# Optimization experiments

Measured on AMD Instinct MI355X. Metric: run time of the kernel, lower is better.

Reference implementation:

```python
import jax, jax.numpy as jnp
import numpy as np

N_EMBED = 384
N_HEADS = 6
HEAD_SIZE = 64


def setup_inputs() -> dict:
    key = jax.random.key(0)
    ks = jax.random.split(key, 6)
    B, T = 16, 1024
    x = jax.random.normal(ks[0], (B, T, N_EMBED), dtype=jnp.float32)
    s = 1.0 / np.sqrt(N_EMBED)
    wq = jax.random.normal(ks[1], (N_HEADS, N_EMBED, HEAD_SIZE), dtype=jnp.float32) * s
    wk = jax.random.normal(ks[2], (N_HEADS, N_EMBED, HEAD_SIZE), dtype=jnp.float32) * s
    wv = jax.random.normal(ks[3], (N_HEADS, N_EMBED, HEAD_SIZE), dtype=jnp.float32) * s
    wp = jax.random.normal(ks[4], (N_EMBED, N_EMBED), dtype=jnp.float32) * s
    bp = jnp.zeros((N_EMBED,), dtype=jnp.float32)
    return {"x": x, "wq": wq, "wk": wk, "wv": wv, "wp": wp, "bp": bp}


def reference(x, wq, wk, wv, wp, bp):
    B, T, C = x.shape
    # per-head projections: [B,H,T,D]
    q = jnp.einsum('btc,hcd->bhtd', x, wq)
    k = jnp.einsum('btc,hcd->bhtd', x, wk)
    v = jnp.einsum('btc,hcd->bhtd', x, wv)
    # NOTE: original scales by 1/sqrt(C) with C = embed dim (384), no causal mask
    scores = jnp.einsum('bhtd,bhsd->bhts', q, k) / jnp.sqrt(jnp.asarray(C, x.dtype))
    weights = jax.nn.softmax(scores, axis=-1)  # dropout = identity (eval)
    out = jnp.einsum('bhts,bhsd->bhtd', weights, v)
    # concat heads -> [B,T,H*D]
    out = out.transpose(0, 2, 1, 3).reshape(B, T, -1)
    return out @ wp.T + bp
```

## Files before the change

### kernel.cpp

```cpp
#include <hip/hip_runtime.h>
#include <hip/hip_bf16.h>

#define Hn 6
#define Tn 1024
#define Cn 384
#define Dn 64
#define Bn 16
#define Mn (Bn*Tn)
#define QSCALE 0.07362222f

typedef __attribute__((ext_vector_type(8)))  short s16x8;
typedef __attribute__((ext_vector_type(16))) float f32x16;

__device__ __forceinline__ void gl_lds16(const void* g, void* l) {
  __builtin_amdgcn_global_load_lds(
      (const __attribute__((address_space(1))) unsigned int*)g,
      (__attribute__((address_space(3))) unsigned int*)l, 16, 0, 0);
}
__device__ __forceinline__ unsigned pk2f(float a, float b) {
  __hip_bfloat162 h = __float22bfloat162_rn(make_float2(a, b));
  union { __hip_bfloat162 h; unsigned u; } cv; cv.h = h; return cv.u;
}
__device__ __forceinline__ f32x16 mfma32(s16x8 a, s16x8 b, f32x16 c) {
  return __builtin_amdgcn_mfma_f32_32x32x16_bf16(a, b, c, 0, 0, 0);
}

__global__ __launch_bounds__(256) void convert_all(
    const float* __restrict__ x, const float* __restrict__ wq,
    const float* __restrict__ wk, const float* __restrict__ wv,
    const float* __restrict__ wp,
    __hip_bfloat16* __restrict__ xb, __hip_bfloat16* __restrict__ wt,
    __hip_bfloat16* __restrict__ wpb)
{
  const int bid = blockIdx.x, t = threadIdx.x;
  if (bid < 18) {
    __shared__ float lt[64][65];
    const int mat = bid / Hn, hh = bid % Hn;
    const float* src = (mat == 0 ? wq : mat == 1 ? wk : wv) + (size_t)hh * (Cn*Dn);
    __hip_bfloat16* dst = wt + (size_t)mat * (Hn*Dn*Cn) + (size_t)hh * (Dn*Cn);
    const float sc = (mat == 0) ? QSCALE : 1.0f;
    for (int ct = 0; ct < 6; ++ct) {
      __syncthreads();
      #pragma unroll
      for (int ps = 0; ps < 4; ++ps) {
        int idx = ps*256 + t;
        int cl = idx >> 4, s4 = idx & 15;
        float4 v = *reinterpret_cast<const float4*>(src + (size_t)(ct*64 + cl)*Dn + s4*4);
        lt[cl][s4*4+0] = v.x * sc; lt[cl][s4*4+1] = v.y * sc;
        lt[cl][s4*4+2] = v.z * sc; lt[cl][s4*4+3] = v.w * sc;
      }
      __syncthreads();
      const int dd = t >> 2, cq = t & 3;
      #pragma unroll
      for (int i = 0; i < 16; ++i)
        dst[(size_t)dd*Cn + ct*64 + cq*16 + i] = __float2bfloat16(lt[cq*16 + i][dd]);
    }
  } else if (bid < 90) {
    const size_t base = (size_t)(bid - 18) * 2048 + (size_t)t * 8;
    float4 a = *reinterpret_cast<const float4*>(wp + base);
    float4 b = *reinterpret_cast<const float4*>(wp + base + 4);
    uint4 r; r.x = pk2f(a.x,a.y); r.y = pk2f(a.z,a.w); r.z = pk2f(b.x,b.y); r.w = pk2f(b.z,b.w);
    *reinterpret_cast<uint4*>((char*)wpb + base*2) = r;
  } else {
    const size_t base = (size_t)(bid - 90) * 2048 + (size_t)t * 8;
    float4 a = *reinterpret_cast<const float4*>(x + base);
    float4 b = *reinterpret_cast<const float4*>(x + base + 4);
    uint4 r; r.x = pk2f(a.x,a.y); r.y = pk2f(a.z,a.w); r.z = pk2f(b.x,b.y); r.w = pk2f(b.z,b.w);
    *reinterpret_cast<uint4*>((char*)xb + base*2) = r;
  }
}

__global__ __launch_bounds__(256) void qkv_proj(
    const __hip_bfloat16* __restrict__ xb, const __hip_bfloat16* __restrict__ wt,
    __hip_bfloat16* __restrict__ qo, __hip_bfloat16* __restrict__ ko,
    __hip_bfloat16* __restrict__ vto)
{
  __shared__ __align__(16) char sm[8192];
  const int t = threadIdx.x, lane = t & 63, w = t >> 6;
  const int hi = lane >> 5, nl = lane & 31;
  const int wr = w >> 1, wc = w & 1;
  const int m0 = blockIdx.x * 64;
  const int mat = blockIdx.y / Hn, h = blockIdx.y % Hn;
  const __hip_bfloat16* wb = wt + (size_t)mat*(Hn*Dn*Cn) + (size_t)h*(Dn*Cn);

  const int mrow = wr*32 + nl;
  const int nrow = wc*32 + nl;
  f32x16 acc = {};
  for (int k0 = 0; k0 < Cn; k0 += 32) {
    __syncthreads();
    #pragma unroll
    for (int c = 0; c < 2; ++c) {
      const int off = w*2048 + c*1024 + lane*16;
      const char* src;
      if (off < 4096) {
        const int row = off >> 6, sl = (off >> 4) & 3;
        src = (const char*)(xb + (size_t)(m0 + row)*Cn + k0) + ((sl ^ (row & 3)) * 16);
      } else {
        const int o2 = off - 4096;
        const int row = o2 >> 6, sl = (o2 >> 4) & 3;
        src = (const char*)(wb + (size_t)row*Cn + k0) + ((sl ^ (row & 3)) * 16);
      }
      gl_lds16(src, sm + w*2048 + c*1024);
    }
    __syncthreads();
    #pragma unroll
    for (int kk = 0; kk < 2; ++kk) {
      s16x8 a  = *reinterpret_cast<const s16x8*>(sm + mrow*64 + (((2*kk + hi) ^ (mrow & 3)) * 16));
      s16x8 bb = *reinterpret_cast<const s16x8*>(sm + 4096 + nrow*64 + (((2*kk + hi) ^ (nrow & 3)) * 16));
      acc = mfma32(a, bb, acc);
    }
  }
  const int d = wc*32 + nl;
  if (mat < 2) {
    __hip_bfloat16* op = (mat == 0) ? qo : ko;
    #pragma unroll
    for (int r = 0; r < 16; ++r) {
      const int ml = wr*32 + (r & 3) + 8*(r >> 2) + 4*hi;
      const int M = m0 + ml, bI = M >> 10, tl = M & 1023;
      op[(((size_t)bI*Hn + h)*Tn + tl)*Dn + d] = __float2bfloat16(acc[r]);
    }
  } else {
    #pragma unroll
    for (int rq = 0; rq < 4; ++rq) {
      const int ml = wr*32 + 8*rq + 4*hi;
      const int M = m0 + ml, bI = M >> 10, tl = M & 1023;
      const unsigned u0 = pk2f(acc[rq*4+0], acc[rq*4+1]);
      const unsigned u1 = pk2f(acc[rq*4+2], acc[rq*4+3]);
      const unsigned long long v = ((unsigned long long)u1 << 32) | u0;
      *reinterpret_cast<unsigned long long*>(
          (char*)vto + ((((size_t)bI*Hn + h)*Dn + d)*Tn + tl)*2) = v;
    }
  }
}

__global__ __launch_bounds__(256) void attn_fwd(
    const __hip_bfloat16* __restrict__ qb, const __hip_bfloat16* __restrict__ kb,
    const __hip_bfloat16* __restrict__ vtb, __hip_bfloat16* __restrict__ ao)
{
  __shared__ __align__(16) char smem[16384];
  const int t = threadIdx.x, lane = t & 63, w = t >> 6;
  const int hi = lane >> 5, qm = lane & 31;
  const int l7 = lane & 7;
  const int bh = blockIdx.x >> 3, qt = blockIdx.x & 7;
  const int b = bh / Hn, h = bh % Hn;

  const int qrow = qt*128 + w*32 + qm;
  const __hip_bfloat16* qrp = qb + ((size_t)bh*Tn + qrow)*Dn;
  s16x8 qf[4];
  #pragma unroll
  for (int hh = 0; hh < 4; ++hh)
    qf[hh] = *reinterpret_cast<const s16x8*>(qrp + hh*16 + hi*8);

  const size_t kbase = (size_t)bh * Tn * Dn;
  const size_t vbase = (size_t)bh * Dn * Tn;

  f32x16 oacc[2] = {};
  float lsum = 0.f;

  for (int kt = 0; kt < 16; ++kt) {
    __syncthreads();
    #pragma unroll
    for (int c = 0; c < 4; ++c) {
      const int off = w*4096 + c*1024 + lane*16;
      const char* src;
      if (off < 8192) {
        const int row = off >> 7, sl = (off >> 4) & 7;
        src = (const char*)(kb + kbase + (size_t)(kt*64 + row)*Dn) + ((sl ^ (row & 7)) * 16);
      } else {
        const int o2 = off - 8192;
        const int row = o2 >> 7, sl = (o2 >> 4) & 7;
        src = (const char*)(vtb + vbase + (size_t)row*Tn + kt*64) + ((sl ^ (row & 7)) * 16);
      }
      gl_lds16(src, smem + w*4096 + c*1024);
    }
    __syncthreads();

    f32x16 sacc[2] = {};
    #pragma unroll
    for (int ts = 0; ts < 2; ++ts) {
      const int srow = ts*32 + qm;
      #pragma unroll
      for (int hh = 0; hh < 4; ++hh) {
        s16x8 ka = *reinterpret_cast<const s16x8*>(
            smem + srow*128 + (((2*hh + hi) ^ l7) * 16));
        sacc[ts] = mfma32(ka, qf[hh], sacc[ts]);
      }
    }
    #pragma unroll
    for (int ts = 0; ts < 2; ++ts)
      #pragma unroll
      for (int r = 0; r < 16; ++r) { float p = exp2f(sacc[ts][r]); sacc[ts][r] = p; lsum += p; }

    #pragma unroll
    for (int m = 0; m < 4; ++m) {
      const int ts = m >> 1, rb = 8*(m & 1);
      const unsigned A0 = pk2f(sacc[ts][rb+0], sacc[ts][rb+1]);
      const unsigned A1 = pk2f(sacc[ts][rb+2], sacc[ts][rb+3]);
      const unsigned B0 = pk2f(sacc[ts][rb+4], sacc[ts][rb+5]);
      const unsigned B1 = pk2f(sacc[ts][rb+6], sacc[ts][rb+7]);
      const unsigned s0 = hi ? A0 : B0;
      const unsigned s1 = hi ? A1 : B1;
      const unsigned r0 = __shfl_xor(s0, 32);
      const unsigned r1 = __shfl_xor(s1, 32);
      union { unsigned u[4]; s16x8 v; } fr;
      fr.u[0] = hi ? r0 : A0;  fr.u[1] = hi ? r1 : A1;
      fr.u[2] = hi ? B0 : r0;  fr.u[3] = hi ? B1 : r1;
      #pragma unroll
      for (int dt = 0; dt < 2; ++dt) {
        const int drow = dt*32 + qm;
        s16x8 va = *reinterpret_cast<const s16x8*>(
            smem + 8192 + drow*128 + (((2*m + hi) ^ l7) * 16));
        oacc[dt] = mfma32(va, fr.v, oacc[dt]);
      }
    }
  }

  lsum += __shfl_xor(lsum, 32);
  const float inv = 1.0f / lsum;

  __syncthreads();
  const int qloc = w*32 + qm;
  #pragma unroll
  for (int dt = 0; dt < 2; ++dt)
    #pragma unroll
    for (int rq = 0; rq < 4; ++rq) {
      const unsigned u0 = pk2f(oacc[dt][rq*4+0]*inv, oacc[dt][rq*4+1]*inv);
      const unsigned u1 = pk2f(oacc[dt][rq*4+2]*inv, oacc[dt][rq*4+3]*inv);
      const unsigned long long v = ((unsigned long long)u1 << 32) | u0;
      *reinterpret_cast<unsigned long long*>(
          smem + qloc*128 + (((4*dt + rq) ^ (qm & 7)) * 16) + 8*hi) = v;
    }
  __syncthreads();
  {
    const int qr = t >> 1, half = t & 1;
    char* dst = (char*)ao + ((size_t)(b*Tn + qt*128 + qr))*(Cn*2) + (h*Dn + half*32)*2;
    #pragma unroll
    for (int sl = 0; sl < 4; ++sl) {
      uint4 v = *reinterpret_cast<const uint4*>(
          smem + qr*128 + (((half*4 + sl) ^ (qr & 7)) * 16));
      *reinterpret_cast<uint4*>(dst + sl*16) = v;
    }
  }
}

__global__ __launch_bounds__(256) void out_proj(
    const __hip_bfloat16* __restrict__ ab, const __hip_bfloat16* __restrict__ wpb,
    const float* __restrict__ bp, float* __restrict__ out)
{
  __shared__ __align__(16) char sm[8192];
  const int t = threadIdx.x, lane = t & 63, w = t >> 6;
  const int hi = lane >> 5, nl = lane & 31;
  const int wr = w >> 1, wc = w & 1;
  const int m0 = blockIdx.x * 64;
  const int n0 = blockIdx.y * 64;

  const int mrow = wr*32 + nl;
  const int nrow = wc*32 + nl;
  f32x16 acc = {};
  for (int k0 = 0; k0 < Cn; k0 += 32) {
    __syncthreads();
    #pragma unroll
    for (int c = 0; c < 2; ++c) {
      const int off = w*2048 + c*1024 + lane*16;
      const char* src;
      if (off < 4096) {
        const int row = off >> 6, sl = (off >> 4) & 3;
        src = (const char*)(ab + (size_t)(m0 + row)*Cn + k0) + ((sl ^ (row & 3)) * 16);
      } else {
        const int o2 = off - 4096;
        const int row = o2 >> 6, sl = (o2 >> 4) & 3;
        src = (const char*)(wpb + (size_t)(n0 + row)*Cn + k0) + ((sl ^ (row & 3)) * 16);
      }
      gl_lds16(src, sm + w*2048 + c*1024);
    }
    __syncthreads();
    #pragma unroll
    for (int kk = 0; kk < 2; ++kk) {
      s16x8 a  = *reinterpret_cast<const s16x8*>(sm + mrow*64 + (((2*kk + hi) ^ (mrow & 3)) * 16));
      s16x8 bb = *reinterpret_cast<const s16x8*>(sm + 4096 + nrow*64 + (((2*kk + hi) ^ (nrow & 3)) * 16));
      acc = mfma32(a, bb, acc);
    }
  }
  const int n = n0 + wc*32 + nl;
  const float bv = bp[n];
  #pragma unroll
  for (int r = 0; r < 16; ++r) {
    const int ml = wr*32 + (r & 3) + 8*(r >> 2) + 4*hi;
    out[(size_t)(m0 + ml)*Cn + n] = acc[r] + bv;
  }
}

extern "C" void kernel_launch(void* const* d_in, const int* in_sizes, int n_in,
                              void* d_out, int out_size, void* d_ws, size_t ws_size,
                              hipStream_t stream) {
  const float* x  = (const float*)d_in[0];
  const float* wq = (const float*)d_in[1];
  const float* wk = (const float*)d_in[2];
  const float* wv = (const float*)d_in[3];
  const float* wp = (const float*)d_in[4];
  const float* bp = (const float*)d_in[5];
  float* out = (float*)d_out;

  unsigned char* W = (unsigned char*)d_ws;
  __hip_bfloat16* xb  = (__hip_bfloat16*)(W);
  __hip_bfloat16* wt  = (__hip_bfloat16*)(W + 12582912);
  __hip_bfloat16* wpb = (__hip_bfloat16*)(W + 13467648);
  __hip_bfloat16* qv  = (__hip_bfloat16*)(W + 13762560);
  __hip_bfloat16* kv  = (__hip_bfloat16*)(W + 26345472);
  __hip_bfloat16* vt  = (__hip_bfloat16*)(W + 38928384);
  __hip_bfloat16* at  = (__hip_bfloat16*)(W + 51511296);

  convert_all<<<3162, 256, 0, stream>>>(x, wq, wk, wv, wp, xb, wt, wpb);
  qkv_proj<<<dim3(Mn/64, 3*Hn), 256, 0, stream>>>(xb, wt, qv, kv, vt);
  attn_fwd<<<Bn*Hn*(Tn/128), 256, 0, stream>>>(qv, kv, vt, at);
  out_proj<<<dim3(Mn/64, Cn/64), 256, 0, stream>>>(at, wpb, bp, out);
}
```

Before: 192.3 us.

## Double-buffer LDS loads in all three kernels with wider K tiles

Adds double-buffered shared-memory staging to the QKV projection, attention and output projection kernels, so global-to-LDS loads for the next tile are issued while MFMAs run on the current one. The GEMM kernels also widen the K step from 32 to 64 and use an 8-way XOR swizzle. Attention blocks are reordered so consecutive blocks cover different heads, and MFMA sections are raised to a higher wave priority. The cost is four times the LDS per GEMM block and twice per attention block, which may lower occupancy.

Result: faster. 183.5 us (-4.6%).

```diff
diff --git a/kernel.cpp b/kernel.cpp
--- a/kernel.cpp
+++ b/kernel.cpp
@@ -75,7 +75,7 @@
     __hip_bfloat16* __restrict__ qo, __hip_bfloat16* __restrict__ ko,
     __hip_bfloat16* __restrict__ vto)
 {
-  __shared__ __align__(16) char sm[8192];
+  __shared__ __align__(16) char sm[32768];
   const int t = threadIdx.x, lane = t & 63, w = t >> 6;
   const int hi = lane >> 5, nl = lane & 31;
   const int wr = w >> 1, wc = w & 1;
@@ -86,30 +86,45 @@
   const int mrow = wr*32 + nl;
   const int nrow = wc*32 + nl;
   f32x16 acc = {};
-  for (int k0 = 0; k0 < Cn; k0 += 32) {
-    __syncthreads();
-    #pragma unroll
-    for (int c = 0; c < 2; ++c) {
-      const int off = w*2048 + c*1024 + lane*16;
+
+  auto stage = [&](int bb, int s) {
+    #pragma unroll
+    for (int c = 0; c < 4; ++c) {
+      const int off = w*4096 + c*1024 + lane*16;
       const char* src;
-      if (off < 4096) {
-        const int row = off >> 6, sl = (off >> 4) & 3;
-        src = (const char*)(xb + (size_t)(m0 + row)*Cn + k0) + ((sl ^ (row & 3)) * 16);
+      if (off < 8192) {
+        const int row = off >> 7, sl = (off >> 4) & 7;
+        src = (const char*)xb + (size_t)(m0 + row)*768 + s*128 + ((sl ^ (row & 7)) * 16);
       } else {
-        const int o2 = off - 4096;
-        const int row = o2 >> 6, sl = (o2 >> 4) & 3;
-        src = (const char*)(wb + (size_t)row*Cn + k0) + ((sl ^ (row & 3)) * 16);
-      }
-      gl_lds16(src, sm + w*2048 + c*1024);
-    }
-    __syncthreads();
-    #pragma unroll
-    for (int kk = 0; kk < 2; ++kk) {
-      s16x8 a  = *reinterpret_cast<const s16x8*>(sm + mrow*64 + (((2*kk + hi) ^ (mrow & 3)) * 16));
-      s16x8 bb = *reinterpret_cast<const s16x8*>(sm + 4096 + nrow*64 + (((2*kk + hi) ^ (nrow & 3)) * 16));
-      acc = mfma32(a, bb, acc);
-    }
-  }
+        const int o2 = off - 8192;
+        const int row = o2 >> 7, sl = (o2 >> 4) & 7;
+        src = (const char*)wb + (size_t)row*768 + s*128 + ((sl ^ (row & 7)) * 16);
+      }
+      gl_lds16(src, sm + bb + w*4096 + c*1024);
+    }
+  };
+  auto compute = [&](int bb) {
+    __builtin_amdgcn_s_setprio(1);
+    #pragma unroll
+    for (int kk = 0; kk < 4; ++kk) {
+      s16x8 a  = *reinterpret_cast<const s16x8*>(sm + bb + mrow*128 + (((2*kk + hi) ^ (mrow & 7)) * 16));
+      s16x8 bv = *reinterpret_cast<const s16x8*>(sm + bb + 8192 + nrow*128 + (((2*kk + hi) ^ (nrow & 7)) * 16));
+      acc = mfma32(a, bv, acc);
+    }
+    __builtin_amdgcn_s_setprio(0);
+  };
+
+  stage(0, 0);
+  __syncthreads();
+  for (int s = 0; s < 6; s += 2) {
+    stage(16384, s + 1);
+    compute(0);
+    __syncthreads();
+    if (s + 2 < 6) stage(0, s + 2);
+    compute(16384);
+    __syncthreads();
+  }
+
   const int d = wc*32 + nl;
   if (mat < 2) {
     __hip_bfloat16* op = (mat == 0) ? qo : ko;
@@ -137,11 +152,12 @@
     const __hip_bfloat16* __restrict__ qb, const __hip_bfloat16* __restrict__ kb,
     const __hip_bfloat16* __restrict__ vtb, __hip_bfloat16* __restrict__ ao)
 {
-  __shared__ __align__(16) char smem[16384];
+  __shared__ __align__(16) char smem[32768];
   const int t = threadIdx.x, lane = t & 63, w = t >> 6;
   const int hi = lane >> 5, qm = lane & 31;
   const int l7 = lane & 7;
-  const int bh = blockIdx.x >> 3, qt = blockIdx.x & 7;
+  const int bx = blockIdx.x;
+  const int bh = bx % 96, qt = bx / 96;
   const int b = bh / Hn, h = bh % Hn;
 
   const int qrow = qt*128 + w*32 + qm;
@@ -157,8 +173,7 @@
   f32x16 oacc[2] = {};
   float lsum = 0.f;
 
-  for (int kt = 0; kt < 16; ++kt) {
-    __syncthreads();
+  auto stage = [&](int bb, int kt) {
     #pragma unroll
     for (int c = 0; c < 4; ++c) {
       const int off = w*4096 + c*1024 + lane*16;
@@ -171,21 +186,24 @@
         const int row = o2 >> 7, sl = (o2 >> 4) & 7;
         src = (const char*)(vtb + vbase + (size_t)row*Tn + kt*64) + ((sl ^ (row & 7)) * 16);
       }
-      gl_lds16(src, smem + w*4096 + c*1024);
-    }
-    __syncthreads();
-
+      gl_lds16(src, smem + bb + w*4096 + c*1024);
+    }
+  };
+
+  auto compute = [&](int bb) {
     f32x16 sacc[2] = {};
+    __builtin_amdgcn_s_setprio(1);
     #pragma unroll
     for (int ts = 0; ts < 2; ++ts) {
       const int srow = ts*32 + qm;
       #pragma unroll
       for (int hh = 0; hh < 4; ++hh) {
         s16x8 ka = *reinterpret_cast<const s16x8*>(
-            smem + srow*128 + (((2*hh + hi) ^ l7) * 16));
+            smem + bb + srow*128 + (((2*hh + hi) ^ l7) * 16));
         sacc[ts] = mfma32(ka, qf[hh], sacc[ts]);
       }
     }
+    __builtin_amdgcn_s_setprio(0);
     #pragma unroll
     for (int ts = 0; ts < 2; ++ts)
       #pragma unroll
@@ -205,20 +223,32 @@
       union { unsigned u[4]; s16x8 v; } fr;
       fr.u[0] = hi ? r0 : A0;  fr.u[1] = hi ? r1 : A1;
       fr.u[2] = hi ? B0 : r0;  fr.u[3] = hi ? B1 : r1;
+      __builtin_amdgcn_s_setprio(1);
       #pragma unroll
       for (int dt = 0; dt < 2; ++dt) {
         const int drow = dt*32 + qm;
         s16x8 va = *reinterpret_cast<const s16x8*>(
-            smem + 8192 + drow*128 + (((2*m + hi) ^ l7) * 16));
+            smem + bb + 8192 + drow*128 + (((2*m + hi) ^ l7) * 16));
         oacc[dt] = mfma32(va, fr.v, oacc[dt]);
       }
-    }
+      __builtin_amdgcn_s_setprio(0);
+    }
+  };
+
+  stage(0, 0);
+  __syncthreads();
+  for (int kt = 0; kt < 16; kt += 2) {
+    stage(16384, kt + 1);
+    compute(0);
+    __syncthreads();
+    if (kt + 2 < 16) stage(0, kt + 2);
+    compute(16384);
+    __syncthreads();
   }
 
   lsum += __shfl_xor(lsum, 32);
   const float inv = 1.0f / lsum;
 
-  __syncthreads();
   const int qloc = w*32 + qm;
   #pragma unroll
   for (int dt = 0; dt < 2; ++dt)
@@ -247,7 +277,7 @@
     const __hip_bfloat16* __restrict__ ab, const __hip_bfloat16* __restrict__ wpb,
     const float* __restrict__ bp, float* __restrict__ out)
 {
-  __shared__ __align__(16) char sm[8192];
+  __shared__ __align__(16) char sm[32768];
   const int t = threadIdx.x, lane = t & 63, w = t >> 6;
   const int hi = lane >> 5, nl = lane & 31;
   const int wr = w >> 1, wc = w & 1;
@@ -257,30 +287,45 @@
   const int mrow = wr*32 + nl;
   const int nrow = wc*32 + nl;
   f32x16 acc = {};
-  for (int k0 = 0; k0 < Cn; k0 += 32) {
-    __syncthreads();
-    #pragma unroll
-    for (int c = 0; c < 2; ++c) {
-      const int off = w*2048 + c*1024 + lane*16;
+
+  auto stage = [&](int bb, int s) {
+    #pragma unroll
+    for (int c = 0; c < 4; ++c) {
+      const int off = w*4096 + c*1024 + lane*16;
       const char* src;
-      if (off < 4096) {
-        const int row = off >> 6, sl = (off >> 4) & 3;
-        src = (const char*)(ab + (size_t)(m0 + row)*Cn + k0) + ((sl ^ (row & 3)) * 16);
+      if (off < 8192) {
+        const int row = off >> 7, sl = (off >> 4) & 7;
+        src = (const char*)ab + (size_t)(m0 + row)*768 + s*128 + ((sl ^ (row & 7)) * 16);
       } else {
-        const int o2 = off - 4096;
-        const int row = o2 >> 6, sl = (o2 >> 4) & 3;
-        src = (const char*)(wpb + (size_t)(n0 + row)*Cn + k0) + ((sl ^ (row & 3)) * 16);
-      }
-      gl_lds16(src, sm + w*2048 + c*1024);
-    }
-    __syncthreads();
-    #pragma unroll
-    for (int kk = 0; kk < 2; ++kk) {
-      s16x8 a  = *reinterpret_cast<const s16x8*>(sm + mrow*64 + (((2*kk + hi) ^ (mrow & 3)) * 16));
-      s16x8 bb = *reinterpret_cast<const s16x8*>(sm + 4096 + nrow*64 + (((2*kk + hi) ^ (nrow & 3)) * 16));
-      acc = mfma32(a, bb, acc);
-    }
-  }
+        const int o2 = off - 8192;
+        const int row = o2 >> 7, sl = (o2 >> 4) & 7;
+        src = (const char*)wpb + (size_t)(n0 + row)*768 + s*128 + ((sl ^ (row & 7)) * 16);
+      }
+      gl_lds16(src, sm + bb + w*4096 + c*1024);
+    }
+  };
+  auto compute = [&](int bb) {
+    __builtin_amdgcn_s_setprio(1);
+    #pragma unroll
+    for (int kk = 0; kk < 4; ++kk) {
+      s16x8 a  = *reinterpret_cast<const s16x8*>(sm + bb + mrow*128 + (((2*kk + hi) ^ (mrow & 7)) * 16));
+      s16x8 bv = *reinterpret_cast<const s16x8*>(sm + bb + 8192 + nrow*128 + (((2*kk + hi) ^ (nrow & 7)) * 16));
+      acc = mfma32(a, bv, acc);
+    }
+    __builtin_amdgcn_s_setprio(0);
+  };
+
+  stage(0, 0);
+  __syncthreads();
+  for (int s = 0; s < 6; s += 2) {
+    stage(16384, s + 1);
+    compute(0);
+    __syncthreads();
+    if (s + 2 < 6) stage(0, s + 2);
+    compute(16384);
+    __syncthreads();
+  }
+
   const int n = n0 + wc*32 + nl;
   const float bv = bp[n];
   #pragma unroll
```
